# Performance work log

Measured on AMD Instinct MI355X. Metric: run time of the kernel, lower is better.

Reference implementation:

```python
import jax, jax.numpy as jnp
import numpy as np

B, C, N = 4, 256, 512
CQ = C // 4
SIGMA = 15.0
PICK = 0  # args.picked_point_num
FACTOR = 180.0 / (np.pi * SIGMA)
BN_EPS = 1e-5


def _angle_embed(angles, W, b):
    """SinusoidalPositionalEmbedding (interleaved sin/cos, detached) + Linear proj."""
    d = W.shape[0]
    div_term = jnp.exp(jnp.arange(0, d, 2, dtype=jnp.float32) * (-np.log(10000.0) / d))
    omegas = (angles * FACTOR)[..., None] * div_term  # (..., d/2)
    # torch cat([sin, cos], dim=2) on (-1, d/2, 1) then view -> interleaved [s0,c0,s1,c1,...]
    emb = jnp.stack([jnp.sin(omegas), jnp.cos(omegas)], axis=-1).reshape(*angles.shape, d)
    emb = jax.lax.stop_gradient(emb)  # .detach() in torch
    return emb @ W.T + b


def setup_inputs() -> dict:
    key = jax.random.key(0)
    ks = jax.random.split(key, 16)
    s = 0.05
    return {
        "x": jax.random.normal(ks[0], (B, C, N), jnp.float32),
        "pca": jax.random.normal(ks[1], (B, C, N), jnp.float32),
        "angle_lrf": jax.random.uniform(ks[2], (B, N, N), jnp.float32, 0.0, np.pi),
        "angle_pca": jax.random.uniform(ks[3], (B, N), jnp.float32, 0.0, np.pi),
        "Wkp": jax.random.normal(ks[4], (CQ, C), jnp.float32) * s,
        "Wk": jax.random.normal(ks[5], (CQ, C), jnp.float32) * s,
        "Wv": jax.random.normal(ks[6], (C, C), jnp.float32) * s,
        "Wvp": jax.random.normal(ks[7], (C, C), jnp.float32) * s,
        "emb1_W": jax.random.normal(ks[8], (CQ, CQ), jnp.float32) * s,
        "emb1_b": jnp.zeros((CQ,), jnp.float32),
        "emb2_W": jax.random.normal(ks[9], (CQ, CQ), jnp.float32) * s,
        "emb2_b": jnp.zeros((CQ,), jnp.float32),
        "lin_W": jax.random.normal(ks[10], (C, C), jnp.float32) * s,
        "lin_b": jnp.zeros((C,), jnp.float32),
        "bn_gamma": jnp.ones((C,), jnp.float32),
        "bn_beta": jnp.zeros((C,), jnp.float32),
    }


def reference(x, pca, angle_lrf, angle_pca, Wkp, Wk, Wv, Wvp,
              emb1_W, emb1_b, emb2_W, emb2_b, lin_W, lin_b, bn_gamma, bn_beta):
    # q uses the k_conv_pca weight (weight tying in __init__)
    x_q = jnp.einsum('oc,bcn->bno', Wkp, x)            # (B,N,CQ)
    k_lrf = jnp.einsum('oc,bcn->bon', Wk, x)           # (B,CQ,N)
    k_pca = jnp.einsum('oc,bcn->bon', Wkp, pca)        # (B,CQ,N)
    energy_lrf = jnp.einsum('bno,bom->bnm', x_q, k_lrf)
    energy_pca = jnp.einsum('bno,bom->bnm', x_q, k_pca)
    e1 = _angle_embed(angle_lrf, emb1_W, emb1_b)       # (B,N,N,CQ) relative-angle bias
    energy_lrf = energy_lrf + jnp.einsum('bnc,bnmc->bnm', x_q, e1)
    e2 = _angle_embed(angle_pca, emb2_W, emb2_b)       # (B,N,CQ)
    energy_pca = energy_pca + jnp.einsum('bnc,bmc->bnm', x_q, e2)
    energy = jax.nn.softmax(energy_lrf + energy_pca, axis=-1)
    # extra column renormalization
    energy = energy / (1e-12 + energy.sum(axis=1, keepdims=True))
    point_relation = energy[:, PICK:PICK + 1, :]       # (B,1,N)
    v_lrf = jnp.einsum('oc,bcn->bon', Wv, x)
    v_pca = jnp.einsum('oc,bcn->bon', Wvp, pca)
    x_lrf = jnp.einsum('bon,bnm->bom', v_lrf, energy)
    x_pca = jnp.einsum('bon,bnm->bom', v_pca, energy)
    x_r = 0.5 * x_lrf + 0.5 * x_pca
    z = jnp.einsum('oc,bcn->bon', lin_W, x - x_r) + lin_b[None, :, None]
    # BatchNorm1d (training-mode batch stats, biased var)
    mu = z.mean(axis=(0, 2), keepdims=True)
    var = z.var(axis=(0, 2), keepdims=True)
    y = bn_gamma[None, :, None] * (z - mu) * jax.lax.rsqrt(var + BN_EPS) + bn_beta[None, :, None]
    out = x + jax.nn.gelu(y, approximate=False)
    return out, point_relation
```

## Files before the change

kernel.cpp:

```cpp
#include <hip/hip_runtime.h>
#include <math.h>

#define FCT_REV 0.6079271018540267f
#define DIVK 0.28782313662425575f
#define INV2PI 0.15915494309189535f

using bf16x8 = __attribute__((ext_vector_type(8))) short;
using f32x4  = __attribute__((ext_vector_type(4))) float;

__device__ inline short f2bf(float f) {
    union { float f; unsigned u; } v; v.f = f;
    unsigned r = v.u + 0x7FFFu + ((v.u >> 16) & 1u);
    return (short)(r >> 16);
}
__device__ inline float bf2f(short s) {
    union { unsigned u; float f; } v;
    v.u = ((unsigned)(unsigned short)s) << 16;
    return v.f;
}
__device__ inline float bflo(unsigned u) {
    union { unsigned q; float f; } v; v.q = u << 16; return v.f;
}
__device__ inline float bfhi(unsigned u) {
    union { unsigned q; float f; } v; v.q = u & 0xFFFF0000u; return v.f;
}
__device__ inline unsigned pk2(float lo, float hi) {
    return ((unsigned)(unsigned short)f2bf(hi) << 16) | (unsigned)(unsigned short)f2bf(lo);
}
__device__ inline float sinrev(float x) {
    float r; asm("v_sin_f32 %0, %1" : "=v"(r) : "v"(x)); return r;
}
__device__ inline float cosrev(float x) {
    float r; asm("v_cos_f32 %0, %1" : "=v"(r) : "v"(x)); return r;
}

__global__ __launch_bounds__(256) void k_prep(
    const float* __restrict__ Wkp, const float* __restrict__ Wk,
    const float* __restrict__ Wv, const float* __restrict__ Wvp,
    const float* __restrict__ linW, const float* __restrict__ e1W,
    const float* __restrict__ e2W,
    const float* __restrict__ x, const float* __restrict__ pca,
    short* __restrict__ Wcatb, short* __restrict__ InTb,
    float* __restrict__ e2Wt, float* __restrict__ stat, float* __restrict__ colsum)
{
    __shared__ float ts[64][65];
    const int bid = blockIdx.x;
    const int t = threadIdx.x;
    if (bid < 176) {
        if (bid == 0) {
            for (int i = t; i < 2048; i += 256) colsum[i] = 0.f;
            for (int i = t; i < 512; i += 256) stat[i] = 0.f;
        } else if (bid == 1) {
            for (int i = t; i < 4096; i += 256) {
                int k = i >> 6, o = i & 63;
                e2Wt[k*64 + o] = e2W[o*64 + k];
            }
        }
        #pragma unroll
        for (int rr = 0; rr < 4; ++rr) {
            const int r = bid*4 + rr;
            for (int k = t; k < 512; k += 256) {
                float v = 0.f;
                if (r < 64) { if (k < 256) v = Wkp[r*256 + k]; }
                else if (r < 128) { int o = r-64;  v = (k<256) ? Wk[o*256+k]  : Wkp[o*256 + k-256]; }
                else if (r < 384) { int o = r-128; v = (k<256) ? Wv[o*256+k]  : Wvp[o*256 + k-256]; }
                else if (r < 640) { int o = r-384; if (k<256) v = linW[o*256+k]; }
                else {
                    int o = r-640;
                    if (k < 256) {
                        float a = 0.f;
                        for (int j = 0; j < 64; ++j) a = fmaf(e1W[j*64 + o], Wkp[j*256 + k], a);
                        v = a;
                    }
                }
                Wcatb[(size_t)r*512 + k] = f2bf(v);
            }
        }
    } else {
        const int id = bid - 176;
        const int b  = id >> 6;
        const int kt = (id >> 3) & 7;
        const int nt = id & 7;
        const int k0 = kt*64, n0 = nt*64;
        const float* src = (k0 < 256) ? (x + ((size_t)b*256 + k0)*512)
                                      : (pca + ((size_t)b*256 + (k0-256))*512);
        #pragma unroll
        for (int i = 0; i < 16; ++i) {
            int idx = t + 256*i;
            int r = idx >> 6, c = idx & 63;
            ts[r][c] = src[(size_t)r*512 + n0 + c];
        }
        __syncthreads();
        short* dst = InTb + (size_t)b*512*512;
        #pragma unroll
        for (int i = 0; i < 16; ++i) {
            int idx = t + 256*i;
            int n = idx >> 6, k = idx & 63;
            dst[(size_t)(n0+n)*512 + k0 + k] = f2bf(ts[k][n]);
        }
    }
}

__global__ __launch_bounds__(256) void k_gemm1(
    const short* __restrict__ Wcatb, const short* __restrict__ InTb,
    const float* __restrict__ angle_pca, const float* __restrict__ e2Wt,
    short* __restrict__ xqb, short* __restrict__ KtT, short* __restrict__ vsumb,
    float* __restrict__ linx, float* __restrict__ q1T)
{
    __shared__ float embs[32][65];
    __shared__ float e2ws[64][64];
    const int bid = blockIdx.x;
    const int b  = bid / 176;
    const int rt = (bid / 16) % 11;
    const int ct = bid % 16;
    const int r0 = rt*64, c0 = ct*32;
    const int w = threadIdx.x >> 6, lane = threadIdx.x & 63;
    const int lr = lane & 15, lg = lane >> 4;
    const int t = threadIdx.x;

    if (r0 == 64) {
        const int mloc = t >> 3, q = t & 7;
        const float arev = angle_pca[b*512 + c0 + mloc] * FCT_REV;
        #pragma unroll
        for (int j = q*4; j < q*4+4; ++j) {
            const float arg = arev * __expf(-(float)j * DIVK);
            embs[mloc][2*j]   = sinrev(arg);
            embs[mloc][2*j+1] = cosrev(arg);
        }
        #pragma unroll
        for (int i = 0; i < 16; ++i) {
            const int idx = t + 256*i;
            e2ws[idx >> 6][idx & 63] = e2Wt[idx];
        }
    }

    const short* ap  = Wcatb + (size_t)(r0 + w*16 + lr)*512 + 8*lg;
    const short* bp0 = InTb + (size_t)b*512*512 + (size_t)(c0 + lr)*512 + 8*lg;
    const short* bp1 = bp0 + 16*512;
    const int kmax = (r0 == 64 || (r0 >= 128 && r0 < 384)) ? 512 : 256;

    f32x4 acc0 = {0.f,0.f,0.f,0.f}, acc1 = {0.f,0.f,0.f,0.f};
    #pragma unroll 4
    for (int kk = 0; kk < kmax; kk += 32) {
        bf16x8 a  = *(const bf16x8*)(ap  + kk);
        bf16x8 b0 = *(const bf16x8*)(bp0 + kk);
        bf16x8 b1 = *(const bf16x8*)(bp1 + kk);
        acc0 = __builtin_amdgcn_mfma_f32_16x16x32_bf16(a, b0, acc0, 0, 0, 0);
        acc1 = __builtin_amdgcn_mfma_f32_16x16x32_bf16(a, b1, acc1, 0, 0, 0);
    }
    const int rowb = r0 + w*16 + lg*4;
    const int col0 = c0 + lr;
    if (r0 == 0) {
        #pragma unroll
        for (int j = 0; j < 4; ++j) {
            xqb[((size_t)b*512 + col0)*64 + rowb + j]      = f2bf(acc0[j]);
            xqb[((size_t)b*512 + col0 + 16)*64 + rowb + j] = f2bf(acc1[j]);
        }
    } else if (r0 == 64) {
        __syncthreads();
        const int o0 = w*16 + lg*4;
        float e[8];
        #pragma unroll
        for (int i = 0; i < 8; ++i) e[i] = 0.f;
        #pragma unroll 8
        for (int k = 0; k < 64; ++k) {
            const float em0 = embs[lr][k];
            const float em1 = embs[lr + 16][k];
            #pragma unroll
            for (int j = 0; j < 4; ++j) {
                const float wv = e2ws[k][o0 + j];
                e[j]     = fmaf(wv, em0, e[j]);
                e[4 + j] = fmaf(wv, em1, e[4 + j]);
            }
        }
        uint2 u0, u1;
        u0.x = pk2(acc0[0] + e[0], acc0[1] + e[1]);
        u0.y = pk2(acc0[2] + e[2], acc0[3] + e[3]);
        u1.x = pk2(acc1[0] + e[4], acc1[1] + e[5]);
        u1.y = pk2(acc1[2] + e[6], acc1[7-3] + e[7]);
        u1.y = pk2(acc1[2] + e[6], acc1[3] + e[7]);
        *(uint2*)(KtT + ((size_t)b*512 + col0)*64 + o0)      = u0;
        *(uint2*)(KtT + ((size_t)b*512 + col0 + 16)*64 + o0) = u1;
    } else if (r0 < 384) {
        #pragma unroll
        for (int j = 0; j < 4; ++j) {
            vsumb[((size_t)b*256 + rowb-128 + j)*512 + col0]      = f2bf(acc0[j]);
            vsumb[((size_t)b*256 + rowb-128 + j)*512 + col0 + 16] = f2bf(acc1[j]);
        }
    } else if (r0 < 640) {
        #pragma unroll
        for (int j = 0; j < 4; ++j) {
            linx[((size_t)b*256 + rowb-384 + j)*512 + col0]      = acc0[j];
            linx[((size_t)b*256 + rowb-384 + j)*512 + col0 + 16] = acc1[j];
        }
    } else {
        const int off = rowb - 640;
        float* d0 = q1T + ((size_t)b*512 + col0)*64 + off;
        float* d1 = q1T + ((size_t)b*512 + col0 + 16)*64 + off;
        d0[0] = sqrtf(acc0[0]*acc0[0] + acc0[1]*acc0[1]);
        d0[1] = atan2f(acc0[1], acc0[0]) * INV2PI;
        d0[2] = sqrtf(acc0[2]*acc0[2] + acc0[3]*acc0[3]);
        d0[3] = atan2f(acc0[3], acc0[2]) * INV2PI;
        d1[0] = sqrtf(acc1[0]*acc1[0] + acc1[1]*acc1[1]);
        d1[1] = atan2f(acc1[1], acc1[0]) * INV2PI;
        d1[2] = sqrtf(acc1[2]*acc1[2] + acc1[3]*acc1[3]);
        d1[3] = atan2f(acc1[3], acc1[2]) * INV2PI;
    }
}

__global__ __launch_bounds__(256) void k_energy3(
    const short* __restrict__ xqb, const short* __restrict__ KtT,
    const float* __restrict__ q1T, const float* __restrict__ angle_lrf,
    short* __restrict__ ETb, float* __restrict__ colsum)
{
    __shared__ short kt[512][68];
    __shared__ float xqf[4][64];
    __shared__ float qs[4][64];
    __shared__ float divs[32];
    __shared__ float4 xw[4];
    const int b  = blockIdx.x >> 7;
    const int n0 = (blockIdx.x & 127) * 4;
    const int t = threadIdx.x;
    {
        const short* src = KtT + (size_t)b*512*64;
        #pragma unroll
        for (int i = 0; i < 16; ++i) {
            const int idx = t + 256*i;
            const int row = idx >> 3, col = (idx & 7) * 8;
            const uint4 u = *(const uint4*)(src + (size_t)row*64 + col);
            *(uint2*)&kt[row][col]     = make_uint2(u.x, u.y);
            *(uint2*)&kt[row][col + 4] = make_uint2(u.z, u.w);
        }
    }
    if (t < 64) {
        #pragma unroll
        for (int i = 0; i < 4; ++i) {
            xqf[i][t] = bf2f(xqb[((size_t)b*512 + n0 + i)*64 + t]);
            qs[i][t]  = q1T[((size_t)b*512 + n0 + i)*64 + t];
        }
    } else if (t < 96) {
        divs[t-64] = __expf(-(float)(t-64) * DIVK);
    }
    __syncthreads();
    float acc[4][2];
    #pragma unroll
    for (int i = 0; i < 4; ++i) { acc[i][0] = 0.f; acc[i][1] = 0.f; }
    for (int c = 0; c < 64; c += 4) {
        float xv[4][4];
        #pragma unroll
        for (int i = 0; i < 4; ++i) {
            #pragma unroll
            for (int j = 0; j < 4; ++j) xv[i][j] = xqf[i][c + j];
        }
        #pragma unroll
        for (int mi = 0; mi < 2; ++mi) {
            const uint2 u = *(const uint2*)&kt[t + mi*256][c];
            const float k0 = bflo(u.x), k1 = bfhi(u.x);
            const float k2 = bflo(u.y), k3 = bfhi(u.y);
            #pragma unroll
            for (int i = 0; i < 4; ++i) {
                acc[i][mi] = fmaf(k0, xv[i][0],
                             fmaf(k1, xv[i][1],
                             fmaf(k2, xv[i][2],
                             fmaf(k3, xv[i][3], acc[i][mi]))));
            }
        }
    }
    float av[4][2];
    #pragma unroll
    for (int i = 0; i < 4; ++i) {
        av[i][0] = angle_lrf[((size_t)b*512 + n0 + i)*512 + t] * FCT_REV;
        av[i][1] = angle_lrf[((size_t)b*512 + n0 + i)*512 + t + 256] * FCT_REV;
    }
    #pragma unroll 2
    for (int j = 0; j < 32; ++j) {
        const float d = divs[j];
        #pragma unroll
        for (int i = 0; i < 4; ++i) {
            const float R = qs[i][2*j], ph = qs[i][2*j+1];
            #pragma unroll
            for (int m = 0; m < 2; ++m) {
                const float arg = fmaf(av[i][m], d, ph);
                acc[i][m] = fmaf(R, sinrev(arg), acc[i][m]);
            }
        }
    }
    float v0 = fmaxf(acc[0][0], acc[0][1]), v1 = fmaxf(acc[1][0], acc[1][1]);
    float v2 = fmaxf(acc[2][0], acc[2][1]), v3 = fmaxf(acc[3][0], acc[3][1]);
    #pragma unroll
    for (int off = 1; off < 64; off <<= 1) {
        v0 = fmaxf(v0, __shfl_xor(v0, off));
        v1 = fmaxf(v1, __shfl_xor(v1, off));
        v2 = fmaxf(v2, __shfl_xor(v2, off));
        v3 = fmaxf(v3, __shfl_xor(v3, off));
    }
    const int wid = t >> 6, lane = t & 63;
    if (lane == 0) { float4 f = {v0,v1,v2,v3}; xw[wid] = f; }
    __syncthreads();
    {
        const float4 a0 = xw[0], a1 = xw[1], a2 = xw[2], a3 = xw[3];
        v0 = fmaxf(fmaxf(a0.x,a1.x), fmaxf(a2.x,a3.x));
        v1 = fmaxf(fmaxf(a0.y,a1.y), fmaxf(a2.y,a3.y));
        v2 = fmaxf(fmaxf(a0.z,a1.z), fmaxf(a2.z,a3.z));
        v3 = fmaxf(fmaxf(a0.w,a1.w), fmaxf(a2.w,a3.w));
    }
    float p[4][2];
    p[0][0] = __expf(acc[0][0]-v0); p[0][1] = __expf(acc[0][1]-v0);
    p[1][0] = __expf(acc[1][0]-v1); p[1][1] = __expf(acc[1][1]-v1);
    p[2][0] = __expf(acc[2][0]-v2); p[2][1] = __expf(acc[2][1]-v2);
    p[3][0] = __expf(acc[3][0]-v3); p[3][1] = __expf(acc[3][1]-v3);
    float s0 = p[0][0]+p[0][1], s1 = p[1][0]+p[1][1];
    float s2 = p[2][0]+p[2][1], s3 = p[3][0]+p[3][1];
    #pragma unroll
    for (int off = 1; off < 64; off <<= 1) {
        s0 += __shfl_xor(s0, off); s1 += __shfl_xor(s1, off);
        s2 += __shfl_xor(s2, off); s3 += __shfl_xor(s3, off);
    }
    __syncthreads();
    if (lane == 0) { float4 f = {s0,s1,s2,s3}; xw[wid] = f; }
    __syncthreads();
    {
        const float4 a0 = xw[0], a1 = xw[1], a2 = xw[2], a3 = xw[3];
        s0 = (a0.x+a1.x) + (a2.x+a3.x);
        s1 = (a0.y+a1.y) + (a2.y+a3.y);
        s2 = (a0.z+a1.z) + (a2.z+a3.z);
        s3 = (a0.w+a1.w) + (a2.w+a3.w);
    }
    const float i0 = 1.f/s0, i1 = 1.f/s1, i2 = 1.f/s2, i3 = 1.f/s3;
    short* Eb = ETb + (size_t)b*512*512;
    #pragma unroll
    for (int mi = 0; mi < 2; ++mi) {
        const int m = t + mi*256;
        const float e0 = p[0][mi]*i0, e1 = p[1][mi]*i1, e2 = p[2][mi]*i2, e3 = p[3][mi]*i3;
        uint2 u;
        u.x = pk2(e0, e1);
        u.y = pk2(e2, e3);
        *(uint2*)(Eb + (size_t)m*512 + n0) = u;
        atomicAdd(&colsum[b*512 + m], (e0 + e1) + (e2 + e3));
    }
}

__global__ __launch_bounds__(256) void k_xr2(
    const short* __restrict__ vsumb, const short* __restrict__ ETb,
    const float* __restrict__ colsum, short* __restrict__ xrT,
    float* __restrict__ out)
{
    const int bid = blockIdx.x;
    const int b  = bid / 64;
    const int rt = (bid / 16) % 4;
    const int ct = bid % 16;
    const int r0 = rt*64, c0 = ct*32;
    const int w = threadIdx.x >> 6, lane = threadIdx.x & 63;
    const int lr = lane & 15, lg = lane >> 4;
    const short* ap  = vsumb + (size_t)b*256*512 + (size_t)(r0 + w*16 + lr)*512 + 8*lg;
    const short* bp0 = ETb + (size_t)b*512*512 + (size_t)(c0 + lr)*512 + 8*lg;
    const short* bp1 = bp0 + 16*512;
    f32x4 acc0 = {0.f,0.f,0.f,0.f}, acc1 = {0.f,0.f,0.f,0.f};
    #pragma unroll 4
    for (int kk = 0; kk < 512; kk += 32) {
        bf16x8 a  = *(const bf16x8*)(ap  + kk);
        bf16x8 b0 = *(const bf16x8*)(bp0 + kk);
        bf16x8 b1 = *(const bf16x8*)(bp1 + kk);
        acc0 = __builtin_amdgcn_mfma_f32_16x16x32_bf16(a, b0, acc0, 0, 0, 0);
        acc1 = __builtin_amdgcn_mfma_f32_16x16x32_bf16(a, b1, acc1, 0, 0, 0);
    }
    const int rowb = r0 + w*16 + lg*4;
    const int m0 = c0 + lr, m1 = m0 + 16;
    const float rc0 = 1.f / (1e-12f + colsum[b*512 + m0]);
    const float rc1 = 1.f / (1e-12f + colsum[b*512 + m1]);
    const float s0 = 0.5f * rc0, s1 = 0.5f * rc1;
    short* xb = xrT + (size_t)b*512*256;
    uint2 u;
    u.x = pk2(acc0[0]*s0, acc0[1]*s0);
    u.y = pk2(acc0[2]*s0, acc0[3]*s0);
    *(uint2*)(xb + (size_t)m0*256 + rowb) = u;
    u.x = pk2(acc1[0]*s1, acc1[1]*s1);
    u.y = pk2(acc1[2]*s1, acc1[3]*s1);
    *(uint2*)(xb + (size_t)m1*256 + rowb) = u;
    if (w == 0 && lg == 0) {
        out[(size_t)4*256*512 + b*512 + m0] = bf2f(ETb[((size_t)b*512 + m0)*512]) * rc0;
        out[(size_t)4*256*512 + b*512 + m1] = bf2f(ETb[((size_t)b*512 + m1)*512]) * rc1;
    }
}

__global__ __launch_bounds__(256) void k_z2st(
    const short* __restrict__ Wcatb, const short* __restrict__ xrT,
    const float* __restrict__ linx, const float* __restrict__ lin_b,
    float* __restrict__ z, float* __restrict__ stat)
{
    const int bid = blockIdx.x;
    const int b  = bid / 64;
    const int rt = (bid / 16) % 4;
    const int ct = bid % 16;
    const int r0 = rt*64, c0 = ct*32;
    const int w = threadIdx.x >> 6, lane = threadIdx.x & 63;
    const int lr = lane & 15, lg = lane >> 4;
    const short* ap  = Wcatb + (size_t)(384 + r0 + w*16 + lr)*512 + 8*lg;
    const short* bp0 = xrT + (size_t)b*512*256 + (size_t)(c0 + lr)*256 + 8*lg;
    const short* bp1 = bp0 + 16*256;
    f32x4 acc0 = {0.f,0.f,0.f,0.f}, acc1 = {0.f,0.f,0.f,0.f};
    #pragma unroll
    for (int kk = 0; kk < 256; kk += 32) {
        bf16x8 a  = *(const bf16x8*)(ap  + kk);
        bf16x8 b0 = *(const bf16x8*)(bp0 + kk);
        bf16x8 b1 = *(const bf16x8*)(bp1 + kk);
        acc0 = __builtin_amdgcn_mfma_f32_16x16x32_bf16(a, b0, acc0, 0, 0, 0);
        acc1 = __builtin_amdgcn_mfma_f32_16x16x32_bf16(a, b1, acc1, 0, 0, 0);
    }
    const int rowb = r0 + w*16 + lg*4;
    const int col0 = c0 + lr;
    const float* Lb = linx + (size_t)b*256*512;
    float* zb = z + (size_t)b*256*512;
    #pragma unroll
    for (int j = 0; j < 4; ++j) {
        const float lb = lin_b[rowb+j];
        const float z0 = Lb[(size_t)(rowb+j)*512 + col0]      - acc0[j] + lb;
        const float z1 = Lb[(size_t)(rowb+j)*512 + col0 + 16] - acc1[j] + lb;
        zb[(size_t)(rowb+j)*512 + col0]      = z0;
        zb[(size_t)(rowb+j)*512 + col0 + 16] = z1;
        float s  = z0 + z1;
        float s2 = z0*z0 + z1*z1;
        #pragma unroll
        for (int off = 1; off < 16; off <<= 1) {
            s  += __shfl_xor(s,  off);
            s2 += __shfl_xor(s2, off);
        }
        if (lr == 0) {
            atomicAdd(&stat[rowb+j], s);
            atomicAdd(&stat[256 + rowb+j], s2);
        }
    }
}

__global__ __launch_bounds__(256) void k_final(
    const float* __restrict__ x, const float* __restrict__ z,
    const float* __restrict__ stat, const float* __restrict__ gamma,
    const float* __restrict__ beta, float* __restrict__ out)
{
    const int gid = blockIdx.x*256 + threadIdx.x;
    const int base = gid * 4;
    const int c = (base >> 9) & 255;
    const float mu  = stat[c] * (1.f/2048.f);
    const float var = stat[256 + c] * (1.f/2048.f) - mu*mu;
    const float gsc = gamma[c] * rsqrtf(var + 1e-5f);
    const float bt  = beta[c];
    const float4 zv = *(const float4*)&z[base];
    const float4 xv = *(const float4*)&x[base];
    float4 ov;
    {
        float y = (zv.x - mu)*gsc + bt;
        ov.x = xv.x + 0.5f*y*(1.f + erff(y*0.70710678118654752f));
        y = (zv.y - mu)*gsc + bt;
        ov.y = xv.y + 0.5f*y*(1.f + erff(y*0.70710678118654752f));
        y = (zv.z - mu)*gsc + bt;
        ov.z = xv.z + 0.5f*y*(1.f + erff(y*0.70710678118654752f));
        y = (zv.w - mu)*gsc + bt;
        ov.w = xv.w + 0.5f*y*(1.f + erff(y*0.70710678118654752f));
    }
    *(float4*)&out[base] = ov;
}

extern "C" void kernel_launch(void* const* d_in, const int* in_sizes, int n_in,
                              void* d_out, int out_size, void* d_ws, size_t ws_size,
                              hipStream_t stream)
{
    const float* x         = (const float*)d_in[0];
    const float* pca       = (const float*)d_in[1];
    const float* angle_lrf = (const float*)d_in[2];
    const float* angle_pca = (const float*)d_in[3];
    const float* Wkp       = (const float*)d_in[4];
    const float* Wk        = (const float*)d_in[5];
    const float* Wv        = (const float*)d_in[6];
    const float* Wvp       = (const float*)d_in[7];
    const float* e1W       = (const float*)d_in[8];
    const float* e2W       = (const float*)d_in[10];
    const float* linW      = (const float*)d_in[12];
    const float* linb      = (const float*)d_in[13];
    const float* gamma     = (const float*)d_in[14];
    const float* beta      = (const float*)d_in[15];

    char* w = (char*)d_ws;
    short* Wcatb  = (short*)(w + 0);
    short* InTb   = (short*)(w + 720896);
    short* vsumb  = (short*)(w + 2818048);
    short* KtT    = (short*)(w + 3866624);
    short* ETb    = (short*)(w + 4128768);
    short* xrT    = (short*)(w + 6225920);
    float* stat   = (float*)(w + 7274496);
    float* colsum = (float*)(w + 7276544);
    float* e2Wt   = (float*)(w + 7284736);
    float* z      = (float*)(w + 7284736);
    short* xqb    = (short*)(w + 12003328);
    float* q1T    = (float*)(w + 12265472);
    float* linx   = (float*)(w + 12789760);
    float* out    = (float*)d_out;

    k_prep   <<<432, 256, 0, stream>>>(Wkp, Wk, Wv, Wvp, linW, e1W, e2W, x, pca,
                                       Wcatb, InTb, e2Wt, stat, colsum);
    k_gemm1  <<<704, 256, 0, stream>>>(Wcatb, InTb, angle_pca, e2Wt,
                                       xqb, KtT, vsumb, linx, q1T);
    k_energy3<<<512, 256, 0, stream>>>(xqb, KtT, q1T, angle_lrf, ETb, colsum);
    k_xr2    <<<256, 256, 0, stream>>>(vsumb, ETb, colsum, xrT, out);
    k_z2st   <<<256, 256, 0, stream>>>(Wcatb, xrT, linx, linb, z, stat);
    k_final  <<<512, 256, 0, stream>>>(x, z, stat, gamma, beta, out);
}
```

Before: 73.20 us.

## Fuse x_r GEMM and lin GEMM into one kernel via shared-memory tile

Merges the k_xr2 and k_z2st kernels into a single k_xrz kernel. Each block computes a 16-column strip of x_r over all 256 channels, keeps it in LDS as bf16, and immediately multiplies it by the lin weights to produce z and the BN statistics. This drops one kernel launch and the xrT round trip through global memory. In exchange the grid shrinks from 256 to 128 blocks, which lowers parallelism, and each block now loops over more A-operand rows. A duplicated dead statement is also removed.

Measured after the change: 89.26 us. 21.9% more time.

```diff
diff --git a/kernel.cpp b/kernel.cpp
--- a/kernel.cpp
+++ b/kernel.cpp
@@ -177,7 +177,6 @@
         u0.x = pk2(acc0[0] + e[0], acc0[1] + e[1]);
         u0.y = pk2(acc0[2] + e[2], acc0[3] + e[3]);
         u1.x = pk2(acc1[0] + e[4], acc1[1] + e[5]);
-        u1.y = pk2(acc1[2] + e[6], acc1[7-3] + e[7]);
         u1.y = pk2(acc1[2] + e[6], acc1[3] + e[7]);
         *(uint2*)(KtT + ((size_t)b*512 + col0)*64 + o0)      = u0;
         *(uint2*)(KtT + ((size_t)b*512 + col0 + 16)*64 + o0) = u1;
@@ -340,94 +339,82 @@
     }
 }
 
-__global__ __launch_bounds__(256) void k_xr2(
+__global__ __launch_bounds__(256) void k_xrz(
     const short* __restrict__ vsumb, const short* __restrict__ ETb,
-    const float* __restrict__ colsum, short* __restrict__ xrT,
-    float* __restrict__ out)
-{
+    const float* __restrict__ colsum, const short* __restrict__ Wcatb,
+    const float* __restrict__ linx, const float* __restrict__ lin_b,
+    float* __restrict__ z, float* __restrict__ stat, float* __restrict__ out)
+{
+    __shared__ short xrs[16][258];
     const int bid = blockIdx.x;
-    const int b  = bid / 64;
-    const int rt = (bid / 16) % 4;
-    const int ct = bid % 16;
-    const int r0 = rt*64, c0 = ct*32;
+    const int b  = bid >> 5;
+    const int m0 = (bid & 31) * 16;
     const int w = threadIdx.x >> 6, lane = threadIdx.x & 63;
     const int lr = lane & 15, lg = lane >> 4;
-    const short* ap  = vsumb + (size_t)b*256*512 + (size_t)(r0 + w*16 + lr)*512 + 8*lg;
-    const short* bp0 = ETb + (size_t)b*512*512 + (size_t)(c0 + lr)*512 + 8*lg;
-    const short* bp1 = bp0 + 16*512;
-    f32x4 acc0 = {0.f,0.f,0.f,0.f}, acc1 = {0.f,0.f,0.f,0.f};
-    #pragma unroll 4
-    for (int kk = 0; kk < 512; kk += 32) {
-        bf16x8 a  = *(const bf16x8*)(ap  + kk);
-        bf16x8 b0 = *(const bf16x8*)(bp0 + kk);
-        bf16x8 b1 = *(const bf16x8*)(bp1 + kk);
-        acc0 = __builtin_amdgcn_mfma_f32_16x16x32_bf16(a, b0, acc0, 0, 0, 0);
-        acc1 = __builtin_amdgcn_mfma_f32_16x16x32_bf16(a, b1, acc1, 0, 0, 0);
-    }
-    const int rowb = r0 + w*16 + lg*4;
-    const int m0 = c0 + lr, m1 = m0 + 16;
-    const float rc0 = 1.f / (1e-12f + colsum[b*512 + m0]);
-    const float rc1 = 1.f / (1e-12f + colsum[b*512 + m1]);
-    const float s0 = 0.5f * rc0, s1 = 0.5f * rc1;
-    short* xb = xrT + (size_t)b*512*256;
-    uint2 u;
-    u.x = pk2(acc0[0]*s0, acc0[1]*s0);
-    u.y = pk2(acc0[2]*s0, acc0[3]*s0);
-    *(uint2*)(xb + (size_t)m0*256 + rowb) = u;
-    u.x = pk2(acc1[0]*s1, acc1[1]*s1);
-    u.y = pk2(acc1[2]*s1, acc1[3]*s1);
-    *(uint2*)(xb + (size_t)m1*256 + rowb) = u;
+
+    {
+        const short* bp = ETb + (size_t)b*512*512 + (size_t)(m0 + lr)*512 + 8*lg;
+        const short* ab = vsumb + (size_t)b*256*512 + 8*lg;
+        f32x4 acc[4] = {{0.f,0.f,0.f,0.f},{0.f,0.f,0.f,0.f},{0.f,0.f,0.f,0.f},{0.f,0.f,0.f,0.f}};
+        for (int kk = 0; kk < 512; kk += 32) {
+            const bf16x8 bfrag = *(const bf16x8*)(bp + kk);
+            #pragma unroll
+            for (int r = 0; r < 4; ++r) {
+                const bf16x8 afrag = *(const bf16x8*)(ab + (size_t)(w*64 + r*16 + lr)*512 + kk);
+                acc[r] = __builtin_amdgcn_mfma_f32_16x16x32_bf16(afrag, bfrag, acc[r], 0, 0, 0);
+            }
+        }
+        const int m = m0 + lr;
+        const float sc = 0.5f / (1e-12f + colsum[b*512 + m]);
+        #pragma unroll
+        for (int r = 0; r < 4; ++r) {
+            const int ob = w*64 + r*16 + lg*4;
+            uint2 u;
+            u.x = pk2(acc[r][0]*sc, acc[r][1]*sc);
+            u.y = pk2(acc[r][2]*sc, acc[r][3]*sc);
+            *(uint2*)&xrs[lr][ob] = u;
+        }
+    }
     if (w == 0 && lg == 0) {
-        out[(size_t)4*256*512 + b*512 + m0] = bf2f(ETb[((size_t)b*512 + m0)*512]) * rc0;
-        out[(size_t)4*256*512 + b*512 + m1] = bf2f(ETb[((size_t)b*512 + m1)*512]) * rc1;
-    }
-}
-
-__global__ __launch_bounds__(256) void k_z2st(
-    const short* __restrict__ Wcatb, const short* __restrict__ xrT,
-    const float* __restrict__ linx, const float* __restrict__ lin_b,
-    float* __restrict__ z, float* __restrict__ stat)
-{
-    const int bid = blockIdx.x;
-    const int b  = bid / 64;
-    const int rt = (bid / 16) % 4;
-    const int ct = bid % 16;
-    const int r0 = rt*64, c0 = ct*32;
-    const int w = threadIdx.x >> 6, lane = threadIdx.x & 63;
-    const int lr = lane & 15, lg = lane >> 4;
-    const short* ap  = Wcatb + (size_t)(384 + r0 + w*16 + lr)*512 + 8*lg;
-    const short* bp0 = xrT + (size_t)b*512*256 + (size_t)(c0 + lr)*256 + 8*lg;
-    const short* bp1 = bp0 + 16*256;
-    f32x4 acc0 = {0.f,0.f,0.f,0.f}, acc1 = {0.f,0.f,0.f,0.f};
-    #pragma unroll
-    for (int kk = 0; kk < 256; kk += 32) {
-        bf16x8 a  = *(const bf16x8*)(ap  + kk);
-        bf16x8 b0 = *(const bf16x8*)(bp0 + kk);
-        bf16x8 b1 = *(const bf16x8*)(bp1 + kk);
-        acc0 = __builtin_amdgcn_mfma_f32_16x16x32_bf16(a, b0, acc0, 0, 0, 0);
-        acc1 = __builtin_amdgcn_mfma_f32_16x16x32_bf16(a, b1, acc1, 0, 0, 0);
-    }
-    const int rowb = r0 + w*16 + lg*4;
-    const int col0 = c0 + lr;
-    const float* Lb = linx + (size_t)b*256*512;
-    float* zb = z + (size_t)b*256*512;
-    #pragma unroll
-    for (int j = 0; j < 4; ++j) {
-        const float lb = lin_b[rowb+j];
-        const float z0 = Lb[(size_t)(rowb+j)*512 + col0]      - acc0[j] + lb;
-        const float z1 = Lb[(size_t)(rowb+j)*512 + col0 + 16] - acc1[j] + lb;
-        zb[(size_t)(rowb+j)*512 + col0]      = z0;
-        zb[(size_t)(rowb+j)*512 + col0 + 16] = z1;
-        float s  = z0 + z1;
-        float s2 = z0*z0 + z1*z1;
-        #pragma unroll
-        for (int off = 1; off < 16; off <<= 1) {
-            s  += __shfl_xor(s,  off);
-            s2 += __shfl_xor(s2, off);
-        }
-        if (lr == 0) {
-            atomicAdd(&stat[rowb+j], s);
-            atomicAdd(&stat[256 + rowb+j], s2);
+        const int m = m0 + lr;
+        const float rc = 1.f / (1e-12f + colsum[b*512 + m]);
+        out[(size_t)4*256*512 + b*512 + m] = bf2f(ETb[((size_t)b*512 + m)*512]) * rc;
+    }
+    __syncthreads();
+
+    {
+        f32x4 acc[4] = {{0.f,0.f,0.f,0.f},{0.f,0.f,0.f,0.f},{0.f,0.f,0.f,0.f},{0.f,0.f,0.f,0.f}};
+        #pragma unroll
+        for (int kk = 0; kk < 256; kk += 32) {
+            const bf16x8 bfrag = *(const bf16x8*)&xrs[lr][8*lg + kk];
+            #pragma unroll
+            for (int r = 0; r < 4; ++r) {
+                const short* ap = Wcatb + (size_t)(384 + w*64 + r*16 + lr)*512 + 8*lg + kk;
+                acc[r] = __builtin_amdgcn_mfma_f32_16x16x32_bf16(*(const bf16x8*)ap, bfrag, acc[r], 0, 0, 0);
+            }
+        }
+        const int col = m0 + lr;
+        float* zb = z + (size_t)b*256*512;
+        const float* Lb = linx + (size_t)b*256*512;
+        #pragma unroll
+        for (int r = 0; r < 4; ++r) {
+            const int cb = w*64 + r*16 + lg*4;
+            #pragma unroll
+            for (int j = 0; j < 4; ++j) {
+                const int c = cb + j;
+                const float zv = Lb[(size_t)c*512 + col] - acc[r][j] + lin_b[c];
+                zb[(size_t)c*512 + col] = zv;
+                float s = zv, s2 = zv*zv;
+                #pragma unroll
+                for (int off = 1; off < 16; off <<= 1) {
+                    s  += __shfl_xor(s,  off);
+                    s2 += __shfl_xor(s2, off);
+                }
+                if (lr == 0) {
+                    atomicAdd(&stat[c], s);
+                    atomicAdd(&stat[256 + c], s2);
+                }
+            }
         }
     }
 }
@@ -485,7 +472,6 @@
     short* vsumb  = (short*)(w + 2818048);
     short* KtT    = (short*)(w + 3866624);
     short* ETb    = (short*)(w + 4128768);
-    short* xrT    = (short*)(w + 6225920);
     float* stat   = (float*)(w + 7274496);
     float* colsum = (float*)(w + 7276544);
     float* e2Wt   = (float*)(w + 7284736);
@@ -500,7 +486,7 @@
     k_gemm1  <<<704, 256, 0, stream>>>(Wcatb, InTb, angle_pca, e2Wt,
                                        xqb, KtT, vsumb, linx, q1T);
     k_energy3<<<512, 256, 0, stream>>>(xqb, KtT, q1T, angle_lrf, ETb, colsum);
-    k_xr2    <<<256, 256, 0, stream>>>(vsumb, ETb, colsum, xrT, out);
-    k_z2st   <<<256, 256, 0, stream>>>(Wcatb, xrT, linx, linb, z, stat);
+    k_xrz    <<<128, 256, 0, stream>>>(vsumb, ETb, colsum, Wcatb, linx, linb,
+                                       z, stat, out);
     k_final  <<<512, 256, 0, stream>>>(x, z, stat, gamma, beta, out);
 }
```
